# Kernel tuning notes

Measured on AMD Instinct MI355X. Metric: run time of the kernel, lower is better.

## Reference

```python
import jax, jax.numpy as jnp
import numpy as np

B, N, C = 2, 4096, 768
H = 12  # num_heads; head_dim = C // H = 64


def setup_inputs() -> dict:
    key = jax.random.key(0)
    kx, kq, kk, kv = jax.random.split(key, 4)
    s = C ** -0.5  # keep param magnitudes sane
    return {
        "x": jax.random.normal(kx, (B, N, C), dtype=jnp.float32),
        "Wq": jax.random.normal(kq, (C, C), dtype=jnp.float32) * s,
        "Wk": jax.random.normal(kk, (C, C), dtype=jnp.float32) * s,
        "Wv": jax.random.normal(kv, (C, C), dtype=jnp.float32) * s,  # created but UNUSED, as in original
    }


def reference(x, Wq, Wk, Wv):
    b, n, c = x.shape
    hd = c // H
    # torch nn.Linear: y = x @ W.T
    q = (x @ Wq.T).reshape(b, n, H, hd).transpose(0, 2, 1, 3)  # [B,H,N,hd]
    k = (x @ Wk.T).reshape(b, n, H, hd).transpose(0, 2, 1, 3)
    # BUG preserved from source: value path uses the K projection, Wv is unused
    v = (x @ Wk.T).reshape(b, n, H, hd).transpose(0, 2, 1, 3)
    # scale by full C (not head_dim), as in source
    attn = jnp.einsum("bhqd,bhkd->bhqk", q, k) * (c ** -0.5)
    attn = jax.nn.softmax(attn, axis=-1)
    out = jnp.einsum("bhqk,bhkd->bhqd", attn, v)  # [B,H,N,hd]
    return out.transpose(0, 2, 1, 3).reshape(b, n, c)
```

## Files before the change

### kernel.cpp

```cpp
#include <hip/hip_runtime.h>

typedef __bf16 bf16;
typedef __bf16 bf16x4 __attribute__((ext_vector_type(4)));
typedef __bf16 bf16x8 __attribute__((ext_vector_type(8)));
typedef float  f32x4  __attribute__((ext_vector_type(4)));
typedef int    int4v  __attribute__((ext_vector_type(4)));

#define NTOK 4096
#define NH   12
#define HD   64
#define CDIM 768

#define K2SCALE 0.05205928442089389f

#define MFMA __builtin_amdgcn_mfma_f32_16x16x32_bf16

__device__ __forceinline__ bf16* swz(bf16* base, int row, int byteoff) {
  return (bf16*)((char*)base + row * 128 +
                 ((((byteoff >> 4) ^ (row & 7)) << 4) | (byteoff & 15)));
}
__device__ __forceinline__ const bf16* swz(const bf16* base, int row, int byteoff) {
  return (const bf16*)((const char*)base + row * 128 +
                 ((((byteoff >> 4) ^ (row & 7)) << 4) | (byteoff & 15)));
}

__global__ __launch_bounds__(256) void cast_kernel(
    const float* __restrict__ x, const float* __restrict__ wq, const float* __restrict__ wk,
    bf16* __restrict__ xb, bf16* __restrict__ wqb, bf16* __restrict__ wkb,
    long nx, long nw) {
  long i4 = ((long)blockIdx.x * 256 + threadIdx.x) * 4;
  if (i4 >= nx + 2 * nw) return;
  const float* src; bf16* dst;
  if (i4 < nx)            { src = x  + i4;            dst = xb  + i4; }
  else if (i4 < nx + nw)  { src = wq + (i4 - nx);     dst = wqb + (i4 - nx); }
  else                    { src = wk + (i4 - nx - nw); dst = wkb + (i4 - nx - nw); }
  f32x4 v = *(const f32x4*)src;
  *(bf16x4*)dst = __builtin_convertvector(v, bf16x4);
}

__global__ __launch_bounds__(256) void proj_kernel(
    const bf16* __restrict__ xb, const bf16* __restrict__ wqb, const bf16* __restrict__ wkb,
    bf16* __restrict__ Qb, bf16* __restrict__ Kb) {
  __shared__ __align__(16) bf16 Ap[128 * 64];
  __shared__ __align__(16) bf16 Bp[128 * 64];
  const int tid = threadIdx.x;
  const int w = tid >> 6, lane = tid & 63, l15 = lane & 15, quad = lane >> 4;
  const int m0 = blockIdx.x * 128;
  const int j0 = blockIdx.y * 128;
  const bf16* W   = blockIdx.z ? wkb : wqb;
  bf16*       Out = blockIdx.z ? Kb  : Qb;
  const float oscale = blockIdx.z ? 1.0f : K2SCALE;

  const int srow = tid >> 3, scb = (tid & 7) * 16, soff = (tid & 7) * 8;
  const bf16* pa = xb + (long)(m0 + srow) * CDIM + soff;
  const bf16* pb = W  + (long)(j0 + srow) * CDIM + soff;

  f32x4 acc[2][8] = {};
  int4v rA[4], rB[4];
#pragma unroll
  for (int i = 0; i < 4; ++i) {
    rA[i] = *(const int4v*)(pa + (long)i * 32 * CDIM);
    rB[i] = *(const int4v*)(pb + (long)i * 32 * CDIM);
  }

  for (int kt = 0; kt < CDIM / 64; ++kt) {
    __syncthreads();
#pragma unroll
    for (int i = 0; i < 4; ++i) {
      *(int4v*)swz(Ap, srow + i * 32, scb) = rA[i];
      *(int4v*)swz(Bp, srow + i * 32, scb) = rB[i];
    }
    __syncthreads();
    const long koff = (long)((kt == CDIM / 64 - 1) ? kt : kt + 1) * 64;
#pragma unroll
    for (int i = 0; i < 4; ++i) {
      rA[i] = *(const int4v*)(pa + (long)i * 32 * CDIM + koff);
      rB[i] = *(const int4v*)(pb + (long)i * 32 * CDIM + koff);
    }
#pragma unroll
    for (int kk = 0; kk < 2; ++kk) {
      bf16x8 a[2], b[8];
#pragma unroll
      for (int rt = 0; rt < 2; ++rt)
        a[rt] = *(const bf16x8*)swz(Ap, w * 32 + rt * 16 + l15, kk * 64 + quad * 16);
#pragma unroll
      for (int ct = 0; ct < 8; ++ct)
        b[ct] = *(const bf16x8*)swz(Bp, ct * 16 + l15, kk * 64 + quad * 16);
#pragma unroll
      for (int rt = 0; rt < 2; ++rt)
#pragma unroll
        for (int ct = 0; ct < 8; ++ct)
          acc[rt][ct] = MFMA(a[rt], b[ct], acc[rt][ct], 0, 0, 0);
    }
  }
#pragma unroll
  for (int rt = 0; rt < 2; ++rt)
#pragma unroll
    for (int ct = 0; ct < 8; ++ct)
#pragma unroll
      for (int reg = 0; reg < 4; ++reg) {
        int m = m0 + w * 32 + rt * 16 + quad * 4 + reg;
        int j = j0 + ct * 16 + l15;
        int b = m >> 12, n = m & (NTOK - 1);
        int h = j >> 6, d = j & (HD - 1);
        Out[(((long)(b * NH + h) * NTOK + n) << 6) + d] = (bf16)(acc[rt][ct][reg] * oscale);
      }
}

__global__ __launch_bounds__(256) void transpose_kernel(
    const bf16* __restrict__ Kb, bf16* __restrict__ Ktb) {
  __shared__ __align__(16) bf16 T[64 * 72];
  const int tid = threadIdx.x;
  const int n0 = blockIdx.x * 64;
  const long bh = blockIdx.y;
#pragma unroll
  for (int i = 0; i < 2; ++i) {
    int c = tid + i * 256;
    int row = c >> 3, off = (c & 7) * 8;
    bf16x8 v = *(const bf16x8*)(Kb + ((bh << 12) + n0 + row) * HD + off);
#pragma unroll
    for (int e = 0; e < 8; ++e) T[(off + e) * 72 + row] = v[e];
  }
  __syncthreads();
#pragma unroll
  for (int i = 0; i < 2; ++i) {
    int c = tid + i * 256;
    int d = c >> 3, koff = (c & 7) * 8;
    int4v v = *(const int4v*)(&T[d * 72 + koff]);
    *(int4v*)(Ktb + ((bh << 6) + d) * (long)NTOK + n0 + koff) = v;
  }
}


#define QKT(SX, MT, KC)                                                        \
  {                                                                            \
    bf16x8 a0 = *(const bf16x8*)swz(KC, (MT) * 16 + l15, quad * 16);           \
    bf16x8 a1 = *(const bf16x8*)swz(KC, (MT) * 16 + l15, 64 + quad * 16);      \
    SX[0] = MFMA(a0, bq[0][0], SX[0], 0, 0, 0);                                \
    SX[1] = MFMA(a0, bq[1][0], SX[1], 0, 0, 0);                                \
    SX[0] = MFMA(a1, bq[0][1], SX[0], 0, 0, 0);                                \
    SX[1] = MFMA(a1, bq[1][1], SX[1], 0, 0, 0);                                \
  }

#define EXP2P(SX, MT)                                                          \
  {                                                                            \
    f32x4 p0, p1;                                                              \
    _Pragma("unroll") for (int r = 0; r < 4; ++r) {                            \
      p0[r] = __builtin_amdgcn_exp2f(SX[0][r]);                                \
      p1[r] = __builtin_amdgcn_exp2f(SX[1][r]);                                \
    }                                                                          \
    lacc[0] += (p0[0] + p0[1]) + (p0[2] + p0[3]);                              \
    lacc[1] += (p1[0] + p1[1]) + (p1[2] + p1[3]);                              \
    *(bf16x4*)swz(QP, w * 32 + l15, (MT) * 32 + quad * 8) =                    \
        __builtin_convertvector(p0, bf16x4);                                   \
    *(bf16x4*)swz(QP, w * 32 + 16 + l15, (MT) * 32 + quad * 8) =               \
        __builtin_convertvector(p1, bf16x4);                                   \
  }

#define PVKK(KK, KTC)                                                          \
  {                                                                            \
    bf16x8 bp0 = *(const bf16x8*)swz(QP, w * 32 + l15, (KK) * 64 + quad * 16); \
    bf16x8 bp1 = *(const bf16x8*)swz(QP, w * 32 + 16 + l15, (KK) * 64 + quad * 16); \
    _Pragma("unroll") for (int mt = 0; mt < 4; ++mt) {                         \
      bf16x8 av = *(const bf16x8*)swz(KTC, mt * 16 + l15, (KK) * 64 + quad * 16); \
      o[mt][0] = MFMA(av, bp0, o[mt][0], 0, 0, 0);                             \
      o[mt][1] = MFMA(av, bp1, o[mt][1], 0, 0, 0);                             \
    }                                                                          \
  }

#define HALF_ITER(C, WK, WT, PK_, PT_, T2)                                     \
  {                                                                            \
    const bf16* Kc  = Ks  + (C) * 4096;                                        \
    const bf16* KTc = Kts + (C) * 4096;                                        \
    bf16* KcW  = Ks  + (1 - (C)) * 4096;                                       \
    bf16* KTcW = Kts + (1 - (C)) * 4096;                                       \
    f32x4 s0[2] = {}, s1[2] = {}, s2[2] = {}, s3[2] = {};                      \
    __builtin_amdgcn_s_setprio(1);                                             \
    QKT(s0, 0, Kc)                                                             \
    QKT(s1, 1, Kc)                                                             \
    *(int4v*)swz(KcW, srow, scb) = WK[0];                                      \
    *(int4v*)swz(KcW, srow + 32, scb) = WK[1];                                 \
    EXP2P(s0, 0)                                                               \
    QKT(s2, 2, Kc)                                                             \
    *(int4v*)swz(KTcW, srow, scb) = WT[0];                                     \
    *(int4v*)swz(KTcW, srow + 32, scb) = WT[1];                                \
    EXP2P(s1, 1)                                                               \
    QKT(s3, 3, Kc)                                                             \
    { const long ko = (long)(T2) * 64;                                         \
      PK_[0] = *(const int4v*)(pk + ko * HD);                                  \
      PK_[1] = *(const int4v*)(pk + (ko + 32) * HD);                           \
      PT_[0] = *(const int4v*)(pkt + ko);                                      \
      PT_[1] = *(const int4v*)(pkt + ko + 32L * NTOK); }                       \
    EXP2P(s2, 2)                                                               \
    EXP2P(s3, 3)                                                               \
    PVKK(0, KTc)                                                               \
    PVKK(1, KTc)                                                               \
    __builtin_amdgcn_s_setprio(0);                                             \
    __syncthreads();                                                           \
  }

__global__ __launch_bounds__(256, 3) void attn_kernel(
    const bf16* __restrict__ Qb, const bf16* __restrict__ Kb, const bf16* __restrict__ Ktb,
    float* __restrict__ out) {
  __shared__ __align__(16) bf16 QP[128 * 64];
  __shared__ __align__(16) bf16 Ks[2 * 64 * 64];
  __shared__ __align__(16) bf16 Kts[2 * 64 * 64];

  const int tid = threadIdx.x;
  const int w = tid >> 6, lane = tid & 63, l15 = lane & 15, quad = lane >> 4;
  const int g = blockIdx.x;
  const int logical = (g & 7) * 96 + (g >> 3);
  const int bh = logical >> 5;
  const int q0 = (logical & 31) * 128;
  const int b = bh / NH, h = bh % NH;
  const bf16* Qhead  = Qb  + (long)bh * NTOK * HD;
  const bf16* Khead  = Kb  + (long)bh * NTOK * HD;
  const bf16* Kthead = Ktb + (long)bh * HD * NTOK;

  const int srow = tid >> 3, scb = (tid & 7) * 16, soff = (tid & 7) * 8;
  const bf16* pk  = Khead  + (long)srow * HD + soff;
  const bf16* pkt = Kthead + (long)srow * NTOK + soff;

#pragma unroll
  for (int i = 0; i < 4; ++i) {
    int c = tid + i * 256;
    int row = c >> 3, cb = (c & 7) * 16;
    int4v v = *(const int4v*)(Qhead + (long)(q0 + row) * HD + (c & 7) * 8);
    *(int4v*)swz(QP, row, cb) = v;
  }

  int4v rAK[2], rAT[2], rBK[2], rBT[2];
  rAK[0] = *(const int4v*)(pk);
  rAK[1] = *(const int4v*)(pk + 32 * HD);
  rAT[0] = *(const int4v*)(pkt);
  rAT[1] = *(const int4v*)(pkt + 32L * NTOK);
  rBK[0] = *(const int4v*)(pk + 64 * HD);
  rBK[1] = *(const int4v*)(pk + 96 * HD);
  rBT[0] = *(const int4v*)(pkt + 64);
  rBT[1] = *(const int4v*)(pkt + 64 + 32L * NTOK);
  *(int4v*)swz(Ks, srow, scb)       = rAK[0];
  *(int4v*)swz(Ks, srow + 32, scb)  = rAK[1];
  *(int4v*)swz(Kts, srow, scb)      = rAT[0];
  *(int4v*)swz(Kts, srow + 32, scb) = rAT[1];
  __syncthreads();

  bf16x8 bq[2][2];
#pragma unroll
  for (int nt = 0; nt < 2; ++nt)
#pragma unroll
    for (int kk = 0; kk < 2; ++kk)
      bq[nt][kk] = *(const bf16x8*)swz(QP, w * 32 + nt * 16 + l15, kk * 64 + quad * 16);

  f32x4 o[4][2] = {};
  float lacc[2] = {0.f, 0.f};

  for (int t = 0; t < NTOK / 64; t += 2) {
    const int n2a = (t + 2 < NTOK / 64) ? t + 2 : NTOK / 64 - 1;
    const int n2b = (t + 3 < NTOK / 64) ? t + 3 : NTOK / 64 - 1;
    HALF_ITER(0, rBK, rBT, rAK, rAT, n2a)
    HALF_ITER(1, rAK, rAT, rBK, rBT, n2b)
  }

#pragma unroll
  for (int nt = 0; nt < 2; ++nt) {
    float l = lacc[nt];
    l += __shfl_xor(l, 16, 64);
    l += __shfl_xor(l, 32, 64);
    float rl = 1.0f / l;
    int n = q0 + w * 32 + nt * 16 + l15;
#pragma unroll
    for (int mt = 0; mt < 4; ++mt) {
      f32x4 v;
#pragma unroll
      for (int reg = 0; reg < 4; ++reg) v[reg] = o[mt][nt][reg] * rl;
      *(f32x4*)(&out[((long)(b * NTOK + n)) * CDIM + h * HD + mt * 16 + quad * 4]) = v;
    }
  }
}

extern "C" void kernel_launch(void* const* d_in, const int* in_sizes, int n_in,
                              void* d_out, int out_size, void* d_ws, size_t ws_size,
                              hipStream_t stream) {
  const float* x  = (const float*)d_in[0];
  const float* Wq = (const float*)d_in[1];
  const float* Wk = (const float*)d_in[2];
  float* out = (float*)d_out;
  char* ws = (char*)d_ws;

  const long NX = (long)2 * NTOK * CDIM;
  const long NW = (long)CDIM * CDIM;

  bf16* xb  = (bf16*)(ws);
  bf16* Ktb = (bf16*)(ws);
  bf16* wqb = (bf16*)(ws + NX * 2);
  bf16* wkb = (bf16*)(ws + NX * 2 + NW * 2);
  bf16* Qb  = (bf16*)(ws + NX * 2 + NW * 4);
  bf16* Kb  = (bf16*)(ws + NX * 2 + NW * 4 + NX * 2);

  long tot4 = (NX + 2 * NW) / 4;
  cast_kernel<<<dim3((tot4 + 255) / 256), 256, 0, stream>>>(x, Wq, Wk, xb, wqb, wkb, NX, NW);
  proj_kernel<<<dim3(8192 / 128, CDIM / 128, 2), 256, 0, stream>>>(xb, wqb, wkb, Qb, Kb);
  transpose_kernel<<<dim3(NTOK / 64, 2 * NH), 256, 0, stream>>>(Kb, Ktb);
  attn_kernel<<<dim3((NTOK / 128) * 2 * NH), 256, 0, stream>>>(Qb, Kb, Ktb, out);
}
```

Before: 242.2 us.

## Software-pipeline PV of previous tile with QK^T of current tile

Restructures the attention main loop so each iteration first runs the P·V MFMAs for the previous key tile and then the QK^T MFMAs for the current tile, with the exp/softmax step placed after both. The goal is to give the exp work independent matrix-core work to overlap with, instead of the P·V step waiting on its own exp results within the same iteration. K and K^T staging are now offset by one tile and use separate double buffers, which needs a peeled first iteration, a special last iteration and an epilogue P·V step. The cost is more code, extra register pressure from the skewed prefetch, and a harder-to-follow buffer-index scheme.

```diff
diff --git a/kernel.cpp b/kernel.cpp
--- a/kernel.cpp
+++ b/kernel.cpp
@@ -168,34 +168,56 @@
     }                                                                          \
   }
 
-#define HALF_ITER(C, WK, WT, PK_, PT_, T2)                                     \
-  {                                                                            \
-    const bf16* Kc  = Ks  + (C) * 4096;                                        \
-    const bf16* KTc = Kts + (C) * 4096;                                        \
+#define ITER(C, PVON, WKS, PKS, WTS, PTS, TK2, TT1)                            \
+  {                                                                            \
+    const bf16* KcR  = Ks  + (C) * 4096;                                       \
+    const bf16* KTcR = Kts + (1 - (C)) * 4096;                                 \
     bf16* KcW  = Ks  + (1 - (C)) * 4096;                                       \
-    bf16* KTcW = Kts + (1 - (C)) * 4096;                                       \
+    bf16* KTcW = Kts + (C) * 4096;                                             \
     f32x4 s0[2] = {}, s1[2] = {}, s2[2] = {}, s3[2] = {};                      \
     __builtin_amdgcn_s_setprio(1);                                             \
-    QKT(s0, 0, Kc)                                                             \
-    QKT(s1, 1, Kc)                                                             \
-    *(int4v*)swz(KcW, srow, scb) = WK[0];                                      \
-    *(int4v*)swz(KcW, srow + 32, scb) = WK[1];                                 \
+    if (PVON) { PVKK(0, KTcR) PVKK(1, KTcR) }                                  \
+    QKT(s0, 0, KcR)                                                            \
+    QKT(s1, 1, KcR)                                                            \
+    QKT(s2, 2, KcR)                                                            \
+    QKT(s3, 3, KcR)                                                            \
+    __builtin_amdgcn_s_setprio(0);                                             \
+    *(int4v*)swz(KcW, srow, scb) = WKS[0];                                     \
+    *(int4v*)swz(KcW, srow + 32, scb) = WKS[1];                                \
+    *(int4v*)swz(KTcW, srow, scb) = WTS[0];                                    \
+    *(int4v*)swz(KTcW, srow + 32, scb) = WTS[1];                               \
     EXP2P(s0, 0)                                                               \
-    QKT(s2, 2, Kc)                                                             \
-    *(int4v*)swz(KTcW, srow, scb) = WT[0];                                     \
-    *(int4v*)swz(KTcW, srow + 32, scb) = WT[1];                                \
     EXP2P(s1, 1)                                                               \
-    QKT(s3, 3, Kc)                                                             \
-    { const long ko = (long)(T2) * 64;                                         \
-      PK_[0] = *(const int4v*)(pk + ko * HD);                                  \
-      PK_[1] = *(const int4v*)(pk + (ko + 32) * HD);                           \
-      PT_[0] = *(const int4v*)(pkt + ko);                                      \
-      PT_[1] = *(const int4v*)(pkt + ko + 32L * NTOK); }                       \
     EXP2P(s2, 2)                                                               \
     EXP2P(s3, 3)                                                               \
-    PVKK(0, KTc)                                                               \
-    PVKK(1, KTc)                                                               \
+    { const long ko = (long)(TK2) * 64;                                        \
+      PKS[0] = *(const int4v*)(pk + ko * HD);                                  \
+      PKS[1] = *(const int4v*)(pk + (ko + 32) * HD); }                         \
+    { const long ko = (long)(TT1) * 64;                                        \
+      PTS[0] = *(const int4v*)(pkt + ko);                                      \
+      PTS[1] = *(const int4v*)(pkt + ko + 32L * NTOK); }                       \
+    __syncthreads();                                                           \
+  }
+
+#define ITER_LAST(WTS)                                                         \
+  {                                                                            \
+    const bf16* KcR  = Ks  + 4096;                                             \
+    const bf16* KTcR = Kts;                                                    \
+    bf16* KTcW = Kts + 4096;                                                   \
+    f32x4 s0[2] = {}, s1[2] = {}, s2[2] = {}, s3[2] = {};                      \
+    __builtin_amdgcn_s_setprio(1);                                             \
+    PVKK(0, KTcR) PVKK(1, KTcR)                                                \
+    QKT(s0, 0, KcR)                                                            \
+    QKT(s1, 1, KcR)                                                            \
+    QKT(s2, 2, KcR)                                                            \
+    QKT(s3, 3, KcR)                                                            \
     __builtin_amdgcn_s_setprio(0);                                             \
+    *(int4v*)swz(KTcW, srow, scb) = WTS[0];                                    \
+    *(int4v*)swz(KTcW, srow + 32, scb) = WTS[1];                               \
+    EXP2P(s0, 0)                                                               \
+    EXP2P(s1, 1)                                                               \
+    EXP2P(s2, 2)                                                               \
+    EXP2P(s3, 3)                                                               \
     __syncthreads();                                                           \
   }
 
@@ -229,19 +251,15 @@
     *(int4v*)swz(QP, row, cb) = v;
   }
 
-  int4v rAK[2], rAT[2], rBK[2], rBT[2];
-  rAK[0] = *(const int4v*)(pk);
-  rAK[1] = *(const int4v*)(pk + 32 * HD);
-  rAT[0] = *(const int4v*)(pkt);
-  rAT[1] = *(const int4v*)(pkt + 32L * NTOK);
-  rBK[0] = *(const int4v*)(pk + 64 * HD);
-  rBK[1] = *(const int4v*)(pk + 96 * HD);
-  rBT[0] = *(const int4v*)(pkt + 64);
-  rBT[1] = *(const int4v*)(pkt + 64 + 32L * NTOK);
-  *(int4v*)swz(Ks, srow, scb)       = rAK[0];
-  *(int4v*)swz(Ks, srow + 32, scb)  = rAK[1];
-  *(int4v*)swz(Kts, srow, scb)      = rAT[0];
-  *(int4v*)swz(Kts, srow + 32, scb) = rAT[1];
+  int4v rK0[2], rK1[2], rKt0[2], rKt1[2];
+  rK0[0]  = *(const int4v*)(pk);
+  rK0[1]  = *(const int4v*)(pk + 32 * HD);
+  rK1[0]  = *(const int4v*)(pk + 64 * HD);
+  rK1[1]  = *(const int4v*)(pk + 96 * HD);
+  rKt0[0] = *(const int4v*)(pkt);
+  rKt0[1] = *(const int4v*)(pkt + 32L * NTOK);
+  *(int4v*)swz(Ks, srow, scb)      = rK0[0];
+  *(int4v*)swz(Ks, srow + 32, scb) = rK0[1];
   __syncthreads();
 
   bf16x8 bq[2][2];
@@ -254,12 +272,23 @@
   f32x4 o[4][2] = {};
   float lacc[2] = {0.f, 0.f};
 
-  for (int t = 0; t < NTOK / 64; t += 2) {
-    const int n2a = (t + 2 < NTOK / 64) ? t + 2 : NTOK / 64 - 1;
-    const int n2b = (t + 3 < NTOK / 64) ? t + 3 : NTOK / 64 - 1;
-    HALF_ITER(0, rBK, rBT, rAK, rAT, n2a)
-    HALF_ITER(1, rAK, rAT, rBK, rBT, n2b)
-  }
+  ITER(0, 0, rK1, rK0, rKt0, rKt1, 2, 1)
+  for (int t = 1; t < 63; t += 2) {
+    const int k2a = t + 2;
+    const int t1a = t + 1;
+    const int k2b = (t + 3 < 64) ? t + 3 : 63;
+    const int t1b = t + 2;
+    ITER(1, 1, rK0, rK1, rKt1, rKt0, k2a, t1a)
+    ITER(0, 1, rK1, rK0, rKt0, rKt1, k2b, t1b)
+  }
+  ITER_LAST(rKt1)
+  __builtin_amdgcn_s_setprio(1);
+  {
+    const bf16* KTcR = Kts + 4096;
+    PVKK(0, KTcR)
+    PVKK(1, KTcR)
+  }
+  __builtin_amdgcn_s_setprio(0);
 
 #pragma unroll
   for (int nt = 0; nt < 2; ++nt) {
```

Result: faster. 235.1 us (-2.9%).

## Switch attention inner loop to 32x32x16 MFMA with register-resident P

Applied to the files above, without the earlier changes.

Replaces the 16x16x32 MFMA tiles for QK^T and PV with 32x32x16 MFMAs. A permuted K row mapping (pl) makes the S accumulator layout match the B-operand layout of the PV MFMA. Probabilities therefore stay in registers instead of round-tripping through the QP shared buffer, which removes LDS writes and reads per tile. The trade-offs are larger f32x16 accumulators that may raise register pressure, and less interleaving of exp work with the MFMAs.

```diff
diff --git a/kernel.cpp b/kernel.cpp
--- a/kernel.cpp
+++ b/kernel.cpp
@@ -4,6 +4,7 @@
 typedef __bf16 bf16x4 __attribute__((ext_vector_type(4)));
 typedef __bf16 bf16x8 __attribute__((ext_vector_type(8)));
 typedef float  f32x4  __attribute__((ext_vector_type(4)));
+typedef float  f32x16 __attribute__((ext_vector_type(16)));
 typedef int    int4v  __attribute__((ext_vector_type(4)));
 
 #define NTOK 4096
@@ -13,7 +14,8 @@
 
 #define K2SCALE 0.05205928442089389f
 
-#define MFMA __builtin_amdgcn_mfma_f32_16x16x32_bf16
+#define MFMA   __builtin_amdgcn_mfma_f32_16x16x32_bf16
+#define MFMA32 __builtin_amdgcn_mfma_f32_32x32x16_bf16
 
 __device__ __forceinline__ bf16* swz(bf16* base, int row, int byteoff) {
   return (bf16*)((char*)base + row * 128 +
@@ -132,69 +134,48 @@
 }
 
 
-#define QKT(SX, MT, KC)                                                        \
+#define ITER(C, WK, WT, PK_, PT_, T2)                                          \
   {                                                                            \
-    bf16x8 a0 = *(const bf16x8*)swz(KC, (MT) * 16 + l15, quad * 16);           \
-    bf16x8 a1 = *(const bf16x8*)swz(KC, (MT) * 16 + l15, 64 + quad * 16);      \
-    SX[0] = MFMA(a0, bq[0][0], SX[0], 0, 0, 0);                                \
-    SX[1] = MFMA(a0, bq[1][0], SX[1], 0, 0, 0);                                \
-    SX[0] = MFMA(a1, bq[0][1], SX[0], 0, 0, 0);                                \
-    SX[1] = MFMA(a1, bq[1][1], SX[1], 0, 0, 0);                                \
-  }
-
-#define EXP2P(SX, MT)                                                          \
-  {                                                                            \
-    f32x4 p0, p1;                                                              \
-    _Pragma("unroll") for (int r = 0; r < 4; ++r) {                            \
-      p0[r] = __builtin_amdgcn_exp2f(SX[0][r]);                                \
-      p1[r] = __builtin_amdgcn_exp2f(SX[1][r]);                                \
-    }                                                                          \
-    lacc[0] += (p0[0] + p0[1]) + (p0[2] + p0[3]);                              \
-    lacc[1] += (p1[0] + p1[1]) + (p1[2] + p1[3]);                              \
-    *(bf16x4*)swz(QP, w * 32 + l15, (MT) * 32 + quad * 8) =                    \
-        __builtin_convertvector(p0, bf16x4);                                   \
-    *(bf16x4*)swz(QP, w * 32 + 16 + l15, (MT) * 32 + quad * 8) =               \
-        __builtin_convertvector(p1, bf16x4);                                   \
-  }
-
-#define PVKK(KK, KTC)                                                          \
-  {                                                                            \
-    bf16x8 bp0 = *(const bf16x8*)swz(QP, w * 32 + l15, (KK) * 64 + quad * 16); \
-    bf16x8 bp1 = *(const bf16x8*)swz(QP, w * 32 + 16 + l15, (KK) * 64 + quad * 16); \
-    _Pragma("unroll") for (int mt = 0; mt < 4; ++mt) {                         \
-      bf16x8 av = *(const bf16x8*)swz(KTC, mt * 16 + l15, (KK) * 64 + quad * 16); \
-      o[mt][0] = MFMA(av, bp0, o[mt][0], 0, 0, 0);                             \
-      o[mt][1] = MFMA(av, bp1, o[mt][1], 0, 0, 0);                             \
-    }                                                                          \
-  }
-
-#define HALF_ITER(C, WK, WT, PK_, PT_, T2)                                     \
-  {                                                                            \
-    const bf16* Kc  = Ks  + (C) * 4096;                                        \
-    const bf16* KTc = Kts + (C) * 4096;                                        \
+    const bf16* KcR  = Ks  + (C) * 4096;                                       \
+    const bf16* KTcR = Kts + (C) * 4096;                                       \
     bf16* KcW  = Ks  + (1 - (C)) * 4096;                                       \
     bf16* KTcW = Kts + (1 - (C)) * 4096;                                       \
-    f32x4 s0[2] = {}, s1[2] = {}, s2[2] = {}, s3[2] = {};                      \
+    f32x16 s0 = {}, s1 = {};                                                   \
     __builtin_amdgcn_s_setprio(1);                                             \
-    QKT(s0, 0, Kc)                                                             \
-    QKT(s1, 1, Kc)                                                             \
+    _Pragma("unroll") for (int ks = 0; ks < 4; ++ks) {                         \
+      bf16x8 a0 = *(const bf16x8*)swz(KcR, pl,      ks * 32 + hh * 16);        \
+      bf16x8 a1 = *(const bf16x8*)swz(KcR, 32 + pl, ks * 32 + hh * 16);        \
+      s0 = MFMA32(a0, bq[ks], s0, 0, 0, 0);                                    \
+      s1 = MFMA32(a1, bq[ks], s1, 0, 0, 0);                                    \
+    }                                                                          \
+    __builtin_amdgcn_s_setprio(0);                                             \
     *(int4v*)swz(KcW, srow, scb) = WK[0];                                      \
     *(int4v*)swz(KcW, srow + 32, scb) = WK[1];                                 \
-    EXP2P(s0, 0)                                                               \
-    QKT(s2, 2, Kc)                                                             \
     *(int4v*)swz(KTcW, srow, scb) = WT[0];                                     \
     *(int4v*)swz(KTcW, srow + 32, scb) = WT[1];                                \
-    EXP2P(s1, 1)                                                               \
-    QKT(s3, 3, Kc)                                                             \
+          \
+    bf16x8 bp[4];                                                              \
+    _Pragma("unroll") for (int ks = 0; ks < 4; ++ks) {                         \
+      bf16x8 t;                                                                \
+      _Pragma("unroll") for (int j = 0; j < 8; ++j) {                          \
+        float p = __builtin_amdgcn_exp2f((ks < 2 ? s0 : s1)[(ks & 1) * 8 + j]);\
+        lacc += p;                                                             \
+        t[j] = (bf16)p;                                                        \
+      }                                                                        \
+      bp[ks] = t;                                                              \
+    }                                                                          \
     { const long ko = (long)(T2) * 64;                                         \
       PK_[0] = *(const int4v*)(pk + ko * HD);                                  \
       PK_[1] = *(const int4v*)(pk + (ko + 32) * HD);                           \
       PT_[0] = *(const int4v*)(pkt + ko);                                      \
       PT_[1] = *(const int4v*)(pkt + ko + 32L * NTOK); }                       \
-    EXP2P(s2, 2)                                                               \
-    EXP2P(s3, 3)                                                               \
-    PVKK(0, KTc)                                                               \
-    PVKK(1, KTc)                                                               \
+    __builtin_amdgcn_s_setprio(1);                                             \
+    _Pragma("unroll") for (int ks = 0; ks < 4; ++ks) {                         \
+      bf16x8 av0 = *(const bf16x8*)swz(KTcR, l31,      ks * 32 + hh * 16);     \
+      bf16x8 av1 = *(const bf16x8*)swz(KTcR, 32 + l31, ks * 32 + hh * 16);     \
+      o0 = MFMA32(av0, bp[ks], o0, 0, 0, 0);                                   \
+      o1 = MFMA32(av1, bp[ks], o1, 0, 0, 0);                                   \
+    }                                                                          \
     __builtin_amdgcn_s_setprio(0);                                             \
     __syncthreads();                                                           \
   }
@@ -207,7 +188,10 @@
   __shared__ __align__(16) bf16 Kts[2 * 64 * 64];
 
   const int tid = threadIdx.x;
-  const int w = tid >> 6, lane = tid & 63, l15 = lane & 15, quad = lane >> 4;
+  const int w = tid >> 6, lane = tid & 63;
+  const int l31 = lane & 31, hh = lane >> 5;
+  const int pl = (l31 & ~12) | ((l31 & 4) << 1) | ((l31 & 8) >> 1);
+
   const int g = blockIdx.x;
   const int logical = (g & 7) * 96 + (g >> 3);
   const int bh = logical >> 5;
@@ -244,36 +228,36 @@
   *(int4v*)swz(Kts, srow + 32, scb) = rAT[1];
   __syncthreads();
 
-  bf16x8 bq[2][2];
-#pragma unroll
-  for (int nt = 0; nt < 2; ++nt)
-#pragma unroll
-    for (int kk = 0; kk < 2; ++kk)
-      bq[nt][kk] = *(const bf16x8*)swz(QP, w * 32 + nt * 16 + l15, kk * 64 + quad * 16);
-
-  f32x4 o[4][2] = {};
-  float lacc[2] = {0.f, 0.f};
+  bf16x8 bq[4];
+#pragma unroll
+  for (int ks = 0; ks < 4; ++ks)
+    bq[ks] = *(const bf16x8*)swz(QP, w * 32 + l31, ks * 32 + hh * 16);
+
+  f32x16 o0 = {}, o1 = {};
+  float lacc = 0.f;
 
   for (int t = 0; t < NTOK / 64; t += 2) {
     const int n2a = (t + 2 < NTOK / 64) ? t + 2 : NTOK / 64 - 1;
     const int n2b = (t + 3 < NTOK / 64) ? t + 3 : NTOK / 64 - 1;
-    HALF_ITER(0, rBK, rBT, rAK, rAT, n2a)
-    HALF_ITER(1, rAK, rAT, rBK, rBT, n2b)
-  }
-
-#pragma unroll
-  for (int nt = 0; nt < 2; ++nt) {
-    float l = lacc[nt];
-    l += __shfl_xor(l, 16, 64);
-    l += __shfl_xor(l, 32, 64);
+    ITER(0, rBK, rBT, rAK, rAT, n2a)
+    ITER(1, rAK, rAT, rBK, rBT, n2b)
+  }
+
+  {
+    float l = lacc + __shfl_xor(lacc, 32, 64);
     float rl = 1.0f / l;
-    int n = q0 + w * 32 + nt * 16 + l15;
-#pragma unroll
-    for (int mt = 0; mt < 4; ++mt) {
-      f32x4 v;
-#pragma unroll
-      for (int reg = 0; reg < 4; ++reg) v[reg] = o[mt][nt][reg] * rl;
-      *(f32x4*)(&out[((long)(b * NTOK + n)) * CDIM + h * HD + mt * 16 + quad * 4]) = v;
+    int n = q0 + w * 32 + l31;
+    float* orow = &out[((long)(b * NTOK + n)) * CDIM + h * HD];
+#pragma unroll
+    for (int gg = 0; gg < 4; ++gg) {
+      f32x4 v0, v1;
+#pragma unroll
+      for (int s = 0; s < 4; ++s) {
+        v0[s] = o0[gg * 4 + s] * rl;
+        v1[s] = o1[gg * 4 + s] * rl;
+      }
+      *(f32x4*)(orow + gg * 8 + hh * 4)      = v0;
+      *(f32x4*)(orow + 32 + gg * 8 + hh * 4) = v1;
     }
   }
 }
```

New measurement: 221.6 us. 8.5% less time.
